# Optimization experiments

Hardware: AMD Instinct MI355X
Metric: run time of the kernel (lower is better)

Reference implementation:

```python
import jax, jax.numpy as jnp
import numpy as np

N_NODES = 100000
N_EDGES = 1600000
D = 128
N_LAYERS = 4
N_GRAPHS = 512


def setup_inputs() -> dict:
    key = jax.random.key(0)
    ks = jax.random.split(key, 12)
    x = jax.random.normal(ks[0], (N_NODES, D), dtype=jnp.float32)
    edge_index = jax.random.randint(ks[1], (2, N_EDGES), 0, N_NODES, dtype=jnp.int64)
    batch = jnp.sort(jax.random.randint(ks[2], (N_NODES,), 0, N_GRAPHS, dtype=jnp.int64))
    scale = 1.0 / np.sqrt(D)
    Ws = jax.random.normal(ks[3], (N_LAYERS, D, D), dtype=jnp.float32) * scale
    bs = jnp.zeros((N_LAYERS, D), dtype=jnp.float32)
    mlp_w1 = jax.random.normal(ks[4], (D, 100), dtype=jnp.float32) * scale
    mlp_b1 = jnp.zeros((100,), dtype=jnp.float32)
    mlp_w2 = jax.random.normal(ks[5], (100, 4), dtype=jnp.float32) * (1.0 / np.sqrt(100.0))
    mlp_b2 = jnp.zeros((4,), dtype=jnp.float32)
    return {"x": x, "Ws": Ws, "bs": bs, "mlp_w1": mlp_w1, "mlp_b1": mlp_b1,
            "mlp_w2": mlp_w2, "mlp_b2": mlp_b2, "edge_index": edge_index, "batch": batch}


def _gcn_conv(x, W, b, row, col, norm):
    # x: [N, Din]; W: [Din, Dout]. PyG GCNConv: linear, then normalized scatter-add.
    xw = x @ W                                # [N, Dout]
    msg = xw[row] * norm[:, None]             # gather at source nodes [E', Dout]
    out = jax.ops.segment_sum(msg, col, num_segments=N_NODES)
    return out + b


def reference(x, Ws, bs, mlp_w1, mlp_b1, mlp_w2, mlp_b2, edge_index, batch):
    # Add self-loops and compute symmetric normalization (once; shared by all layers).
    loop = jnp.arange(N_NODES, dtype=edge_index.dtype)
    row = jnp.concatenate([edge_index[0], loop])  # source
    col = jnp.concatenate([edge_index[1], loop])  # target
    deg = jax.ops.segment_sum(jnp.ones_like(col, dtype=x.dtype), col, num_segments=N_NODES)
    dinv = jnp.where(deg > 0, jax.lax.rsqrt(deg), 0.0)
    norm = dinv[row] * dinv[col]              # [E']

    h = x
    for i in range(N_LAYERS - 1):
        # dropout is identity in eval mode
        h = _gcn_conv(h, Ws[i], bs[i], row, col, norm)
        h = jax.nn.relu(h)
    h = _gcn_conv(h, Ws[-1], bs[-1], row, col, norm)

    # global mean pool over graphs
    sums = jax.ops.segment_sum(h, batch, num_segments=N_GRAPHS)
    counts = jax.ops.segment_sum(jnp.ones((N_NODES,), dtype=h.dtype), batch, num_segments=N_GRAPHS)
    pooled = sums / jnp.maximum(counts, 1.0)[:, None]  # [G, D]

    # MLP head: D -> 100 -> 4 (relu between, dropout identity in eval)
    hid = jax.nn.relu(pooled @ mlp_w1 + mlp_b1)
    pred = hid @ mlp_w2 + mlp_b2
    return pred
```

## Files before the change

kernel.cpp:

```cpp
#include <hip/hip_runtime.h>

#define N_NODES  100000
#define N_EDGES  1600000
#define DIM      128
#define N_GRAPHS 512

#define BW       512
#define NBUCK    ((N_NODES + BW - 1) / BW)
#define CAP      12288
#define NB_CHUNK 4096

typedef short  bf16x8 __attribute__((ext_vector_type(8)));
typedef float  f32x4  __attribute__((ext_vector_type(4)));

__device__ inline ushort f2bf(float f) {
    union { float f; unsigned u; } v; v.f = f;
    unsigned r = v.u + 0x7FFFu + ((v.u >> 16) & 1u);
    return (ushort)(r >> 16);
}
__device__ inline float bf2f_lo(unsigned u) { union { unsigned u; float f; } v; v.u = u << 16; return v.f; }
__device__ inline float bf2f_hi(unsigned u) { union { unsigned u; float f; } v; v.u = u & 0xFFFF0000u; return v.f; }


__global__ __launch_bounds__(256) void cvt_x(const float* __restrict__ x,
                                             const float* __restrict__ dinv,
                                             ushort* __restrict__ xb) {
    int i = (blockIdx.x * 256 + threadIdx.x) * 4;
    float d = dinv[i >> 7];
    float4 v = *(const float4*)(x + i);
    ushort4 o;
    o.x = f2bf(v.x * d); o.y = f2bf(v.y * d); o.z = f2bf(v.z * d); o.w = f2bf(v.w * d);
    *(ushort4*)(xb + i) = o;
}

__global__ __launch_bounds__(256) void cvt_w(const float* __restrict__ Ws,
                                             ushort* __restrict__ WT) {
    int idx = blockIdx.x * 256 + threadIdx.x;
    int L = idx >> 14, n = (idx >> 7) & 127, k = idx & 127;
    WT[idx] = f2bf(Ws[(L << 14) + (k << 7) + n]);
}


__global__ __launch_bounds__(256) void initb_kernel(int* __restrict__ bfill,
                                                    int* __restrict__ csr) {
    int t = threadIdx.x;
    if (t < NBUCK) bfill[t] = t * CAP;
    if (t == 255) csr[N_NODES] = N_EDGES;
}

__global__ __launch_bounds__(256) void bin_kernel(const int* __restrict__ row,
                                                  const int* __restrict__ col,
                                                  int* __restrict__ bfill,
                                                  unsigned* __restrict__ tmp) {
    __shared__ unsigned s_val[NB_CHUNK];
    __shared__ int s_dst[NB_CHUNK];
    __shared__ int s_hist[256], s_scan[256];
    __shared__ int s_excl[NBUCK], s_base[NBUCK], s_cur[NBUCK];
    int t = threadIdx.x;
    int e0 = blockIdx.x * NB_CHUNK;

    s_hist[t] = 0;
    __syncthreads();
#pragma unroll
    for (int k = 0; k < NB_CHUNK / 256; ++k) {
        int e = e0 + t + k * 256;
        if (e < N_EDGES) atomicAdd(&s_hist[col[e] >> 9], 1);
    }
    __syncthreads();
    int h = s_hist[t];
    s_scan[t] = h;
    __syncthreads();
    for (int o = 1; o < 256; o <<= 1) {
        int u = (t >= o) ? s_scan[t - o] : 0;
        __syncthreads();
        s_scan[t] += u;
        __syncthreads();
    }
    if (t < NBUCK) {
        int ex = s_scan[t] - h;
        s_excl[t] = ex;
        s_cur[t]  = ex;
        s_base[t] = atomicAdd(&bfill[t], h);
    }
    __syncthreads();
#pragma unroll
    for (int k = 0; k < NB_CHUNK / 256; ++k) {
        int e = e0 + t + k * 256;
        if (e < N_EDGES) {
            int r = row[e], c = col[e];
            int b = c >> 9;
            int p = atomicAdd(&s_cur[b], 1);
            int dst = s_base[b] + (p - s_excl[b]);
            int lim = (b + 1) * CAP;
            if (dst >= lim) dst = lim - 1;
            s_val[p] = ((unsigned)(c & (BW - 1)) << 17) | (unsigned)r;
            s_dst[p] = dst;
        }
    }
    __syncthreads();
    int sc = N_EDGES - e0; if (sc > NB_CHUNK) sc = NB_CHUNK;
#pragma unroll
    for (int k = 0; k < NB_CHUNK / 256; ++k) {
        int j = t + k * 256;
        if (j < sc) tmp[s_dst[j]] = s_val[j];
    }
}

__global__ __launch_bounds__(256) void bscan_kernel(const int* __restrict__ bfill,
                                                    int* __restrict__ bbase) {
    __shared__ int s[256];
    int t = threadIdx.x;
    int cnt = 0;
    if (t < NBUCK) {
        cnt = bfill[t] - t * CAP;
        if (cnt > CAP) cnt = CAP;
    }
    s[t] = cnt;
    __syncthreads();
    for (int o = 1; o < 256; o <<= 1) {
        int u = (t >= o) ? s[t - o] : 0;
        __syncthreads();
        s[t] += u;
        __syncthreads();
    }
    if (t < NBUCK) bbase[t] = s[t] - cnt;
}

__global__ __launch_bounds__(256) void sort_kernel(const unsigned* __restrict__ tmp,
                                                   const int* __restrict__ bfill,
                                                   const int* __restrict__ bbase,
                                                   int* __restrict__ csr,
                                                   float* __restrict__ dinv,
                                                   int* __restrict__ ssrc) {
    __shared__ int s_cnt[BW];
    __shared__ int s_pair[256];
    __shared__ int s_off[BW];
    __shared__ int s_cur[BW];
    __shared__ int s_stage[CAP];
    int b = blockIdx.x, t = threadIdx.x;
    int wbeg = b * BW;
    int wn = N_NODES - wbeg; if (wn > BW) wn = BW;
    int nE = bfill[b] - b * CAP; if (nE > CAP) nE = CAP;
    const unsigned* T = tmp + (size_t)b * CAP;
    int base = bbase[b];

    for (int i = t; i < BW; i += 256) s_cnt[i] = 0;
    __syncthreads();
    for (int i = t; i < nE; i += 256) atomicAdd(&s_cnt[T[i] >> 17], 1);
    __syncthreads();
    int a0 = s_cnt[2 * t], a1 = s_cnt[2 * t + 1];
    s_pair[t] = a0 + a1;
    __syncthreads();
    for (int o = 1; o < 256; o <<= 1) {
        int u = (t >= o) ? s_pair[t - o] : 0;
        __syncthreads();
        s_pair[t] += u;
        __syncthreads();
    }
    int pre = s_pair[t] - (a0 + a1);
    s_off[2 * t] = pre;      s_off[2 * t + 1] = pre + a0;
    s_cur[2 * t] = pre;      s_cur[2 * t + 1] = pre + a0;
    __syncthreads();
    for (int i = t; i < wn; i += 256) {
        csr[wbeg + i]  = base + s_off[i];
        dinv[wbeg + i] = rsqrtf((float)(s_cnt[i] + 1));
    }
    for (int i = t; i < nE; i += 256) {
        unsigned v = T[i];
        int p = atomicAdd(&s_cur[v >> 17], 1);
        s_stage[p] = (int)(v & 0x1FFFFu);
    }
    __syncthreads();
    for (int i = t; i < nE; i += 256) ssrc[base + i] = s_stage[i];
}

__global__ __launch_bounds__(256) void bounds_kernel(const int* __restrict__ batch,
                                                     int* __restrict__ gstart) {
    int i = blockIdx.x * 256 + threadIdx.x;
    if (i >= N_NODES) return;
    int b  = batch[i];
    int bp = (i == 0) ? -1 : batch[i - 1];
    for (int g = bp + 1; g <= b; ++g) gstart[g] = i;
    if (i == N_NODES - 1) {
        for (int g = b + 1; g <= N_GRAPHS; ++g) gstart[g] = N_NODES;
    }
}

#define ACC8(vv) do { \
    acc[0] += bf2f_lo((vv).x); acc[1] += bf2f_hi((vv).x); \
    acc[2] += bf2f_lo((vv).y); acc[3] += bf2f_hi((vv).y); \
    acc[4] += bf2f_lo((vv).z); acc[5] += bf2f_hi((vv).z); \
    acc[6] += bf2f_lo((vv).w); acc[7] += bf2f_hi((vv).w); } while (0)

__global__ __launch_bounds__(256) void agg_kernel(const ushort* __restrict__ g,
                                                  ushort* __restrict__ out,
                                                  const int* __restrict__ off,
                                                  const int* __restrict__ ssrc,
                                                  const float* __restrict__ dinv) {
    int node = blockIdx.x * 16 + (threadIdx.x >> 4);
    int l    = threadIdx.x & 15;
    const uint4* hp = (const uint4*)g;

    uint4 v = hp[(size_t)node * 16 + l];
    float acc[8];
    acc[0] = bf2f_lo(v.x); acc[1] = bf2f_hi(v.x);
    acc[2] = bf2f_lo(v.y); acc[3] = bf2f_hi(v.y);
    acc[4] = bf2f_lo(v.z); acc[5] = bf2f_hi(v.z);
    acc[6] = bf2f_lo(v.w); acc[7] = bf2f_hi(v.w);

    int e = off[node], end = off[node + 1];
    for (; e + 7 < end; e += 8) {
        int s0 = ssrc[e],     s1 = ssrc[e + 1], s2 = ssrc[e + 2], s3 = ssrc[e + 3];
        int s4 = ssrc[e + 4], s5 = ssrc[e + 5], s6 = ssrc[e + 6], s7 = ssrc[e + 7];
        uint4 v0 = hp[(size_t)s0 * 16 + l];
        uint4 v1 = hp[(size_t)s1 * 16 + l];
        uint4 v2 = hp[(size_t)s2 * 16 + l];
        uint4 v3 = hp[(size_t)s3 * 16 + l];
        uint4 v4 = hp[(size_t)s4 * 16 + l];
        uint4 v5 = hp[(size_t)s5 * 16 + l];
        uint4 v6 = hp[(size_t)s6 * 16 + l];
        uint4 v7 = hp[(size_t)s7 * 16 + l];
        ACC8(v0); ACC8(v1); ACC8(v2); ACC8(v3);
        ACC8(v4); ACC8(v5); ACC8(v6); ACC8(v7);
    }
    for (; e + 1 < end; e += 2) {
        int s0 = ssrc[e], s1 = ssrc[e + 1];
        uint4 v0 = hp[(size_t)s0 * 16 + l];
        uint4 v1 = hp[(size_t)s1 * 16 + l];
        ACC8(v0); ACC8(v1);
    }
    if (e < end) {
        int s = ssrc[e];
        uint4 v1 = hp[(size_t)s * 16 + l];
        ACC8(v1);
    }

    float d = dinv[node];
    uint4 ov;
    ov.x = (uint)f2bf(acc[0] * d) | ((uint)f2bf(acc[1] * d) << 16);
    ov.y = (uint)f2bf(acc[2] * d) | ((uint)f2bf(acc[3] * d) << 16);
    ov.z = (uint)f2bf(acc[4] * d) | ((uint)f2bf(acc[5] * d) << 16);
    ov.w = (uint)f2bf(acc[6] * d) | ((uint)f2bf(acc[7] * d) << 16);
    ((uint4*)out)[(size_t)node * 16 + l] = ov;
}

#define WPAD 136
__global__ __launch_bounds__(256) void gemm_mfma(const ushort* __restrict__ A,
                                                 const ushort* __restrict__ WT,
                                                 const float* __restrict__ bias,
                                                 const float* __restrict__ dinv,
                                                 ushort* __restrict__ out,
                                                 int mode) {
    __shared__ ushort sW[128 * WPAD];
    int t = threadIdx.x;
    {
#pragma unroll
        for (int j = 0; j < 8; ++j) {
            int idx = t + j * 256;
            int r = idx >> 4, qq = idx & 15;
            uint4 v = *(const uint4*)(WT + (size_t)r * 128 + qq * 8);
            *(uint4*)(sW + (size_t)r * WPAD + qq * 8) = v;
        }
    }
    __syncthreads();

    int lane = t & 63;
    int wv   = t >> 6;
    int m0   = blockIdx.x * 128 + wv * 32;
    int l15  = lane & 15;
    int kq   = (lane >> 4) * 8;
    int r0 = m0 + l15, r1 = m0 + 16 + l15;
    if (r0 >= N_NODES) r0 = N_NODES - 1;
    if (r1 >= N_NODES) r1 = N_NODES - 1;

    f32x4 acc0[8], acc1[8];
#pragma unroll
    for (int n = 0; n < 8; ++n) {
        acc0[n] = (f32x4){0.f, 0.f, 0.f, 0.f};
        acc1[n] = (f32x4){0.f, 0.f, 0.f, 0.f};
    }

#pragma unroll
    for (int k0 = 0; k0 < 128; k0 += 32) {
        bf16x8 a0 = *(const bf16x8*)(A + (size_t)r0 * 128 + k0 + kq);
        bf16x8 a1 = *(const bf16x8*)(A + (size_t)r1 * 128 + k0 + kq);
#pragma unroll
        for (int n = 0; n < 8; ++n) {
            bf16x8 b = *(const bf16x8*)(sW + (size_t)(n * 16 + l15) * WPAD + k0 + kq);
            acc0[n] = __builtin_amdgcn_mfma_f32_16x16x32_bf16(a0, b, acc0[n], 0, 0, 0);
            acc1[n] = __builtin_amdgcn_mfma_f32_16x16x32_bf16(a1, b, acc1[n], 0, 0, 0);
        }
    }

#pragma unroll
    for (int sub = 0; sub < 2; ++sub) {
        int orow = m0 + sub * 16 + (lane >> 4) * 4;
        float sc[4];
#pragma unroll
        for (int r = 0; r < 4; ++r) {
            int m = orow + r;
            sc[r] = (mode && m < N_NODES) ? dinv[m] : 1.0f;
        }
#pragma unroll
        for (int n = 0; n < 8; ++n) {
            int col = n * 16 + l15;
            float bv = bias[col];
            f32x4 av = sub ? acc1[n] : acc0[n];
#pragma unroll
            for (int r = 0; r < 4; ++r) {
                int m = orow + r;
                if (m < N_NODES) {
                    float v = av[r] + bv;
                    if (mode) v = fmaxf(v, 0.f) * sc[r];
                    out[(size_t)m * 128 + col] = f2bf(v);
                }
            }
        }
    }
}


__global__ __launch_bounds__(256) void pool_mlp(const ushort* __restrict__ h,
                                                const int* __restrict__ gstart,
                                                const float* __restrict__ w1,
                                                const float* __restrict__ b1,
                                                const float* __restrict__ w2,
                                                const float* __restrict__ b2,
                                                float* __restrict__ out) {
    __shared__ float part[4][128];
    __shared__ float mean[128];
    __shared__ float hid[100];
    int g = blockIdx.x;
    int s = gstart[g], e2 = gstart[g + 1];
    int p     = threadIdx.x & 63;
    int which = threadIdx.x >> 6;
    const uint* hu = (const uint*)h;

    float a0 = 0.f, a1 = 0.f;
    for (int n = s + which; n < e2; n += 4) {
        uint v = hu[(size_t)n * 64 + p];
        a0 += bf2f_lo(v);
        a1 += bf2f_hi(v);
    }
    part[which][2 * p]     = a0;
    part[which][2 * p + 1] = a1;
    __syncthreads();
    if (which == 0) {
        float c = fmaxf((float)(e2 - s), 1.0f);
        mean[2 * p]     = (part[0][2 * p] + part[1][2 * p] + part[2][2 * p] + part[3][2 * p]) / c;
        mean[2 * p + 1] = (part[0][2 * p + 1] + part[1][2 * p + 1] + part[2][2 * p + 1] + part[3][2 * p + 1]) / c;
    }
    __syncthreads();
    int t = threadIdx.x;
    if (t < 100) {
        float s1 = b1[t];
        for (int k = 0; k < 128; ++k) s1 = fmaf(mean[k], w1[k * 100 + t], s1);
        hid[t] = fmaxf(s1, 0.f);
    }
    __syncthreads();
    if (t < 4) {
        float s2 = b2[t];
        for (int j = 0; j < 100; ++j) s2 = fmaf(hid[j], w2[j * 4 + t], s2);
        out[(size_t)g * 4 + t] = s2;
    }
}


extern "C" void kernel_launch(void* const* d_in, const int* in_sizes, int n_in,
                              void* d_out, int out_size, void* d_ws, size_t ws_size,
                              hipStream_t stream) {
    const float* x   = (const float*)d_in[0];
    const float* Ws  = (const float*)d_in[1];
    const float* bs  = (const float*)d_in[2];
    const float* w1  = (const float*)d_in[3];
    const float* b1  = (const float*)d_in[4];
    const float* w2  = (const float*)d_in[5];
    const float* b2  = (const float*)d_in[6];
    const int*   ei  = (const int*)d_in[7];
    const int*   bat = (const int*)d_in[8];
    float* outp = (float*)d_out;

    char* p = (char*)d_ws;
    auto take = [&](size_t bytes) -> void* {
        void* r = (void*)p;
        p += (bytes + 255) & ~(size_t)255;
        return r;
    };
    int*      csr    = (int*)take((size_t)(N_NODES + 1) * 4);
    float*    dinv   = (float*)take((size_t)N_NODES * 4);
    int*      bfill  = (int*)take((size_t)NBUCK * 4);
    int*      bbase  = (int*)take((size_t)NBUCK * 4);
    unsigned* tmp    = (unsigned*)take((size_t)NBUCK * CAP * 4);
    int*      ssrc   = (int*)take((size_t)N_EDGES * 4);
    ushort*   xb     = (ushort*)take((size_t)N_NODES * 128 * 2);
    ushort*   hb     = (ushort*)take((size_t)N_NODES * 128 * 2);
    ushort*   aggb   = (ushort*)take((size_t)N_NODES * 128 * 2);
    ushort*   WT     = (ushort*)take((size_t)4 * 128 * 128 * 2);
    int*      gstart = (int*)take((size_t)(N_GRAPHS + 1) * 4);

    const int* row = ei;
    const int* col = ei + N_EDGES;

    initb_kernel<<<1, 256, 0, stream>>>(bfill, csr);
    bin_kernel<<<(N_EDGES + NB_CHUNK - 1) / NB_CHUNK, 256, 0, stream>>>(row, col, bfill, tmp);
    bscan_kernel<<<1, 256, 0, stream>>>(bfill, bbase);
    sort_kernel<<<NBUCK, 256, 0, stream>>>(tmp, bfill, bbase, csr, dinv, ssrc);
    cvt_x<<<12500, 256, 0, stream>>>(x, dinv, xb);
    cvt_w<<<256, 256, 0, stream>>>(Ws, WT);
    bounds_kernel<<<(N_NODES + 255) / 256, 256, 0, stream>>>(bat, gstart);

    const ushort* hin = xb;
    for (int L = 0; L < 4; ++L) {
        agg_kernel<<<N_NODES / 16, 256, 0, stream>>>(hin, aggb, csr, ssrc, dinv);
        gemm_mfma<<<(N_NODES + 127) / 128, 256, 0, stream>>>(
            aggb, WT + (size_t)L * 128 * 128, bs + (size_t)L * 128, dinv, hb, (L < 3) ? 1 : 0);
        hin = hb;
    }
    pool_mlp<<<N_GRAPHS, 256, 0, stream>>>(hb, gstart, w1, b1, w2, b2, outp);
}
```

Baseline: 519.7 us.

## Widen CSR build blocks, shorten aggregation unroll, stage GEMM output through LDS

The bin and sort kernels now run 1024 threads per block instead of 256, giving each block more parallelism for the edge binning and per-bucket sort. The aggregation gather loop drops from 8-way to 4-way unrolling, which lowers register pressure at the cost of fewer loads in flight. The GEMM epilogue writes bf16 results into the shared weight tile, then stores full 16-byte rows coalesced instead of scattered 2-byte writes. This adds two barriers and reuses the LDS buffer after the MFMA loop.

```diff
diff --git a/kernel.cpp b/kernel.cpp
--- a/kernel.cpp
+++ b/kernel.cpp
@@ -48,10 +48,10 @@
     if (t == 255) csr[N_NODES] = N_EDGES;
 }
 
-__global__ __launch_bounds__(256) void bin_kernel(const int* __restrict__ row,
-                                                  const int* __restrict__ col,
-                                                  int* __restrict__ bfill,
-                                                  unsigned* __restrict__ tmp) {
+__global__ __launch_bounds__(1024) void bin_kernel(const int* __restrict__ row,
+                                                   const int* __restrict__ col,
+                                                   int* __restrict__ bfill,
+                                                   unsigned* __restrict__ tmp) {
     __shared__ unsigned s_val[NB_CHUNK];
     __shared__ int s_dst[NB_CHUNK];
     __shared__ int s_hist[256], s_scan[256];
@@ -59,21 +59,22 @@
     int t = threadIdx.x;
     int e0 = blockIdx.x * NB_CHUNK;
 
-    s_hist[t] = 0;
-    __syncthreads();
-#pragma unroll
-    for (int k = 0; k < NB_CHUNK / 256; ++k) {
-        int e = e0 + t + k * 256;
+    if (t < 256) s_hist[t] = 0;
+    __syncthreads();
+#pragma unroll
+    for (int k = 0; k < 4; ++k) {
+        int e = e0 + t + k * 1024;
         if (e < N_EDGES) atomicAdd(&s_hist[col[e] >> 9], 1);
     }
     __syncthreads();
-    int h = s_hist[t];
-    s_scan[t] = h;
+    int h = 0;
+    if (t < 256) { h = s_hist[t]; s_scan[t] = h; }
     __syncthreads();
     for (int o = 1; o < 256; o <<= 1) {
-        int u = (t >= o) ? s_scan[t - o] : 0;
-        __syncthreads();
-        s_scan[t] += u;
+        int u = 0;
+        if (t < 256 && t >= o) u = s_scan[t - o];
+        __syncthreads();
+        if (t < 256) s_scan[t] += u;
         __syncthreads();
     }
     if (t < NBUCK) {
@@ -84,8 +85,8 @@
     }
     __syncthreads();
 #pragma unroll
-    for (int k = 0; k < NB_CHUNK / 256; ++k) {
-        int e = e0 + t + k * 256;
+    for (int k = 0; k < 4; ++k) {
+        int e = e0 + t + k * 1024;
         if (e < N_EDGES) {
             int r = row[e], c = col[e];
             int b = c >> 9;
@@ -100,8 +101,8 @@
     __syncthreads();
     int sc = N_EDGES - e0; if (sc > NB_CHUNK) sc = NB_CHUNK;
 #pragma unroll
-    for (int k = 0; k < NB_CHUNK / 256; ++k) {
-        int j = t + k * 256;
+    for (int k = 0; k < 4; ++k) {
+        int j = t + k * 1024;
         if (j < sc) tmp[s_dst[j]] = s_val[j];
     }
 }
@@ -126,12 +127,12 @@
     if (t < NBUCK) bbase[t] = s[t] - cnt;
 }
 
-__global__ __launch_bounds__(256) void sort_kernel(const unsigned* __restrict__ tmp,
-                                                   const int* __restrict__ bfill,
-                                                   const int* __restrict__ bbase,
-                                                   int* __restrict__ csr,
-                                                   float* __restrict__ dinv,
-                                                   int* __restrict__ ssrc) {
+__global__ __launch_bounds__(1024) void sort_kernel(const unsigned* __restrict__ tmp,
+                                                    const int* __restrict__ bfill,
+                                                    const int* __restrict__ bbase,
+                                                    int* __restrict__ csr,
+                                                    float* __restrict__ dinv,
+                                                    int* __restrict__ ssrc) {
     __shared__ int s_cnt[BW];
     __shared__ int s_pair[256];
     __shared__ int s_off[BW];
@@ -144,34 +145,37 @@
     const unsigned* T = tmp + (size_t)b * CAP;
     int base = bbase[b];
 
-    for (int i = t; i < BW; i += 256) s_cnt[i] = 0;
-    __syncthreads();
-    for (int i = t; i < nE; i += 256) atomicAdd(&s_cnt[T[i] >> 17], 1);
-    __syncthreads();
-    int a0 = s_cnt[2 * t], a1 = s_cnt[2 * t + 1];
-    s_pair[t] = a0 + a1;
+    for (int i = t; i < BW; i += 1024) s_cnt[i] = 0;
+    __syncthreads();
+    for (int i = t; i < nE; i += 1024) atomicAdd(&s_cnt[T[i] >> 17], 1);
+    __syncthreads();
+    int a0 = 0, a1 = 0;
+    if (t < 256) { a0 = s_cnt[2 * t]; a1 = s_cnt[2 * t + 1]; s_pair[t] = a0 + a1; }
     __syncthreads();
     for (int o = 1; o < 256; o <<= 1) {
-        int u = (t >= o) ? s_pair[t - o] : 0;
-        __syncthreads();
-        s_pair[t] += u;
-        __syncthreads();
-    }
-    int pre = s_pair[t] - (a0 + a1);
-    s_off[2 * t] = pre;      s_off[2 * t + 1] = pre + a0;
-    s_cur[2 * t] = pre;      s_cur[2 * t + 1] = pre + a0;
-    __syncthreads();
-    for (int i = t; i < wn; i += 256) {
+        int u = 0;
+        if (t < 256 && t >= o) u = s_pair[t - o];
+        __syncthreads();
+        if (t < 256) s_pair[t] += u;
+        __syncthreads();
+    }
+    if (t < 256) {
+        int pre = s_pair[t] - (a0 + a1);
+        s_off[2 * t] = pre;      s_off[2 * t + 1] = pre + a0;
+        s_cur[2 * t] = pre;      s_cur[2 * t + 1] = pre + a0;
+    }
+    __syncthreads();
+    for (int i = t; i < wn; i += 1024) {
         csr[wbeg + i]  = base + s_off[i];
         dinv[wbeg + i] = rsqrtf((float)(s_cnt[i] + 1));
     }
-    for (int i = t; i < nE; i += 256) {
+    for (int i = t; i < nE; i += 1024) {
         unsigned v = T[i];
         int p = atomicAdd(&s_cur[v >> 17], 1);
         s_stage[p] = (int)(v & 0x1FFFFu);
     }
     __syncthreads();
-    for (int i = t; i < nE; i += 256) ssrc[base + i] = s_stage[i];
+    for (int i = t; i < nE; i += 1024) ssrc[base + i] = s_stage[i];
 }
 
 __global__ __launch_bounds__(256) void bounds_kernel(const int* __restrict__ batch,
@@ -209,25 +213,20 @@
     acc[6] = bf2f_lo(v.w); acc[7] = bf2f_hi(v.w);
 
     int e = off[node], end = off[node + 1];
-    for (; e + 7 < end; e += 8) {
-        int s0 = ssrc[e],     s1 = ssrc[e + 1], s2 = ssrc[e + 2], s3 = ssrc[e + 3];
-        int s4 = ssrc[e + 4], s5 = ssrc[e + 5], s6 = ssrc[e + 6], s7 = ssrc[e + 7];
+    for (; e + 3 < end; e += 4) {
+        int s0 = ssrc[e], s1 = ssrc[e + 1], s2 = ssrc[e + 2], s3 = ssrc[e + 3];
         uint4 v0 = hp[(size_t)s0 * 16 + l];
         uint4 v1 = hp[(size_t)s1 * 16 + l];
         uint4 v2 = hp[(size_t)s2 * 16 + l];
         uint4 v3 = hp[(size_t)s3 * 16 + l];
-        uint4 v4 = hp[(size_t)s4 * 16 + l];
-        uint4 v5 = hp[(size_t)s5 * 16 + l];
-        uint4 v6 = hp[(size_t)s6 * 16 + l];
-        uint4 v7 = hp[(size_t)s7 * 16 + l];
         ACC8(v0); ACC8(v1); ACC8(v2); ACC8(v3);
-        ACC8(v4); ACC8(v5); ACC8(v6); ACC8(v7);
-    }
-    for (; e + 1 < end; e += 2) {
+    }
+    if (e + 1 < end) {
         int s0 = ssrc[e], s1 = ssrc[e + 1];
         uint4 v0 = hp[(size_t)s0 * 16 + l];
         uint4 v1 = hp[(size_t)s1 * 16 + l];
         ACC8(v0); ACC8(v1);
+        e += 2;
     }
     if (e < end) {
         int s = ssrc[e];
@@ -253,6 +252,7 @@
                                                  int mode) {
     __shared__ ushort sW[128 * WPAD];
     int t = threadIdx.x;
+    int m0blk = blockIdx.x * 128;
     {
 #pragma unroll
         for (int j = 0; j < 8; ++j) {
@@ -266,7 +266,7 @@
 
     int lane = t & 63;
     int wv   = t >> 6;
-    int m0   = blockIdx.x * 128 + wv * 32;
+    int m0   = m0blk + wv * 32;
     int l15  = lane & 15;
     int kq   = (lane >> 4) * 8;
     int r0 = m0 + l15, r1 = m0 + 16 + l15;
@@ -292,29 +292,41 @@
         }
     }
 
-#pragma unroll
-    for (int sub = 0; sub < 2; ++sub) {
-        int orow = m0 + sub * 16 + (lane >> 4) * 4;
-        float sc[4];
-#pragma unroll
-        for (int r = 0; r < 4; ++r) {
-            int m = orow + r;
-            sc[r] = (mode && m < N_NODES) ? dinv[m] : 1.0f;
-        }
-#pragma unroll
-        for (int n = 0; n < 8; ++n) {
-            int col = n * 16 + l15;
-            float bv = bias[col];
-            f32x4 av = sub ? acc1[n] : acc0[n];
+    __syncthreads();
+    {
+        int wrow0 = wv * 32;
+#pragma unroll
+        for (int sub = 0; sub < 2; ++sub) {
+            int rbase = wrow0 + sub * 16 + (lane >> 4) * 4;
+            float sc[4];
 #pragma unroll
             for (int r = 0; r < 4; ++r) {
-                int m = orow + r;
-                if (m < N_NODES) {
+                int m = m0blk + rbase + r;
+                sc[r] = (mode && m < N_NODES) ? dinv[m] : 1.0f;
+            }
+#pragma unroll
+            for (int n = 0; n < 8; ++n) {
+                int col = n * 16 + l15;
+                float bv = bias[col];
+                f32x4 av = sub ? acc1[n] : acc0[n];
+#pragma unroll
+                for (int r = 0; r < 4; ++r) {
                     float v = av[r] + bv;
                     if (mode) v = fmaxf(v, 0.f) * sc[r];
-                    out[(size_t)m * 128 + col] = f2bf(v);
+                    sW[(size_t)(rbase + r) * WPAD + col] = f2bf(v);
                 }
             }
+        }
+    }
+    __syncthreads();
+#pragma unroll
+    for (int j = 0; j < 8; ++j) {
+        int idx = t + j * 256;
+        int rowrel = idx >> 4, qq = idx & 15;
+        int m = m0blk + rowrel;
+        if (m < N_NODES) {
+            uint4 v = *(const uint4*)(sW + (size_t)rowrel * WPAD + qq * 8);
+            *(uint4*)(out + (size_t)m * 128 + qq * 8) = v;
         }
     }
 }
@@ -402,9 +414,9 @@
     const int* col = ei + N_EDGES;
 
     initb_kernel<<<1, 256, 0, stream>>>(bfill, csr);
-    bin_kernel<<<(N_EDGES + NB_CHUNK - 1) / NB_CHUNK, 256, 0, stream>>>(row, col, bfill, tmp);
+    bin_kernel<<<(N_EDGES + NB_CHUNK - 1) / NB_CHUNK, 1024, 0, stream>>>(row, col, bfill, tmp);
     bscan_kernel<<<1, 256, 0, stream>>>(bfill, bbase);
-    sort_kernel<<<NBUCK, 256, 0, stream>>>(tmp, bfill, bbase, csr, dinv, ssrc);
+    sort_kernel<<<NBUCK, 1024, 0, stream>>>(tmp, bfill, bbase, csr, dinv, ssrc);
     cvt_x<<<12500, 256, 0, stream>>>(x, dinv, xb);
     cvt_w<<<256, 256, 0, stream>>>(Ws, WT);
     bounds_kernel<<<(N_NODES + 255) / 256, 256, 0, stream>>>(bat, gstart);
```

After: 475.4 us. -8.5%, faster.
